# Optimization experiments

Hardware: AMD Instinct MI355X
Metric: run time of the kernel (lower is better)

Reference implementation:

```python
import jax, jax.numpy as jnp
import numpy as np

B, S, S2, NH, H, NKEYS = 2, 4096, 2048, 8, 64, 64


def setup_inputs() -> dict:
    key = jax.random.key(0)
    kq, kk, kv, ki = jax.random.split(key, 4)
    q = jax.random.normal(kq, (B, S2, NH, H), dtype=jnp.float32)
    k = jax.random.normal(kk, (B, S, NH, H), dtype=jnp.float32)
    v = jax.random.normal(kv, (B, S, NH, H), dtype=jnp.float32)
    indices_select = jax.random.randint(ki, (B, S2, NKEYS), 0, S, dtype=jnp.int64)
    return {"q": q, "k": k, "v": v, "indices_select": indices_select}


def reference(q, k, v, indices_select):
    b, s, nh, h = k.shape
    q = q * (h ** -0.5)
    # gather n random keys/values per (batch, query): (b, s2, n, nh, h)
    batch_idx = jnp.arange(b)[:, None, None]
    k_g = k[batch_idx, indices_select]
    v_g = v[batch_idx, indices_select]
    # scores over the n gathered keys, per head: (b, q, k, n)
    A = jnp.einsum('bqnh,bqknh->bqkn', q, k_g)
    A = jax.nn.softmax(A, axis=-2)  # softmax over gathered-key dim (torch dim=-2)
    z = jnp.einsum('bqkn,bqknh->bqnh', A, v_g)
    return z
```

## Files before the change

### kernel.cpp

```cpp
#include <hip/hip_runtime.h>


#define BB 2
#define SS 4096
#define S2V 2048
#define NHV 8
#define HV 64
#define NKV 64

__global__ __launch_bounds__(256)
__attribute__((amdgpu_waves_per_eu(4, 4)))
void rsa_kernel(const float* __restrict__ q, const float* __restrict__ k,
                const float* __restrict__ v, const int* __restrict__ idx,
                float* __restrict__ out) {
    const int lane = threadIdx.x & 63;
    const int w    = threadIdx.x >> 6;
    const int bi   = blockIdx.x;

    const int combo = bi & 15;
    const int b     = combo >> 3;
    const int n     = combo & 7;
    const int qi    = ((bi >> 4) << 2) + w;

    const int g  = lane >> 4;
    const int hc = lane & 15;

    const size_t bq = (size_t)b * S2V + qi;

    const float* qrow = q + (bq * NHV + n) * HV;
    const float4 qv = *(const float4*)(qrow + hc * 4);
    const float4 q4 = make_float4(qv.x * 0.125f, qv.y * 0.125f,
                                  qv.z * 0.125f, qv.w * 0.125f);

    const int my_off = idx[bq * NKV + lane] * (NHV * HV);

    const float* kb = k + ((size_t)b * SS * NHV + n) * HV;
    const float* vb = v + ((size_t)b * SS * NHV + n) * HV;

    float4 kr[16];
#pragma unroll
    for (int it = 0; it < 16; ++it) {
        const int off = __shfl(my_off, it * 4 + g, 64);
        kr[it] = *(const float4*)(kb + off + hc * 4);
    }

    float sc[16];
#pragma unroll
    for (int it = 0; it < 16; ++it) {
        float d = kr[it].x * q4.x + kr[it].y * q4.y
                + kr[it].z * q4.z + kr[it].w * q4.w;
        d += __shfl_xor(d, 1);
        d += __shfl_xor(d, 2);
        d += __shfl_xor(d, 4);
        d += __shfl_xor(d, 8);
        sc[it] = d;
    }

    float4 vr[16];
#pragma unroll
    for (int it = 0; it < 16; ++it) {
        const int off = __shfl(my_off, it * 4 + g, 64);
        vr[it] = *(const float4*)(vb + off + hc * 4);
    }

    float m = sc[0];
#pragma unroll
    for (int it = 1; it < 16; ++it) m = fmaxf(m, sc[it]);
    m = fmaxf(m, __shfl_xor(m, 16));
    m = fmaxf(m, __shfl_xor(m, 32));

    float ssum = 0.f;
#pragma unroll
    for (int it = 0; it < 16; ++it) {
        sc[it] = __expf(sc[it] - m);
        ssum += sc[it];
    }
    ssum += __shfl_xor(ssum, 16);
    ssum += __shfl_xor(ssum, 32);
    const float rs = __frcp_rn(ssum);

    float4 z = make_float4(0.f, 0.f, 0.f, 0.f);
#pragma unroll
    for (int it = 0; it < 16; ++it) {
        const float p = sc[it];
        z.x = fmaf(p, vr[it].x, z.x);
        z.y = fmaf(p, vr[it].y, z.y);
        z.z = fmaf(p, vr[it].z, z.z);
        z.w = fmaf(p, vr[it].w, z.w);
    }
    z.x += __shfl_xor(z.x, 16); z.y += __shfl_xor(z.y, 16);
    z.z += __shfl_xor(z.z, 16); z.w += __shfl_xor(z.w, 16);
    z.x += __shfl_xor(z.x, 32); z.y += __shfl_xor(z.y, 32);
    z.z += __shfl_xor(z.z, 32); z.w += __shfl_xor(z.w, 32);

    if (g == 0) {
        float4 zo = make_float4(z.x * rs, z.y * rs, z.z * rs, z.w * rs);
        *(float4*)(out + (bq * NHV + n) * HV + hc * 4) = zo;
    }
}

extern "C" void kernel_launch(void* const* d_in, const int* in_sizes, int n_in,
                              void* d_out, int out_size, void* d_ws, size_t ws_size,
                              hipStream_t stream) {
    const float* q   = (const float*)d_in[0];
    const float* k   = (const float*)d_in[1];
    const float* v   = (const float*)d_in[2];
    const int*   idx = (const int*)d_in[3];
    float*       out = (float*)d_out;

    const int n_units = BB * S2V * NHV;
    const int blocks  = n_units / 4;
    rsa_kernel<<<blocks, 256, 0, stream>>>(q, k, v, idx, out);
}
```

Measured before the change: 123.8 us.

## Convert K/V to fp16 in workspace before the gather-attention kernel

Adds a pre-pass kernel that converts K and V to fp16 in the workspace buffer. The attention kernel then gathers half-width rows, with 8 lanes per key and 8 elements per lane, and accumulates in fp32. This halves the bytes moved by the random gathers, which dominate the cost. In exchange it adds an extra full read and write pass over K and V every call, and introduces fp16 rounding on the keys and values. A restructured fp32 fallback, which interleaves loads with compute, runs only when the workspace is too small.

```diff
diff --git a/kernel.cpp b/kernel.cpp
--- a/kernel.cpp
+++ b/kernel.cpp
@@ -1,4 +1,5 @@
 #include <hip/hip_runtime.h>
+#include <stdint.h>
 
 
 #define BB 2
@@ -8,11 +9,29 @@
 #define HV 64
 #define NKV 64
 
+typedef _Float16 half_t;
+typedef _Float16 half8 __attribute__((ext_vector_type(8)));
+
+#define NE ((size_t)BB * SS * NHV * HV)
+
 __global__ __launch_bounds__(256)
-__attribute__((amdgpu_waves_per_eu(4, 4)))
-void rsa_kernel(const float* __restrict__ q, const float* __restrict__ k,
-                const float* __restrict__ v, const int* __restrict__ idx,
-                float* __restrict__ out) {
+void cvt_kernel(const float* __restrict__ k, const float* __restrict__ v,
+                half_t* __restrict__ kh, half_t* __restrict__ vh) {
+    const size_t base = ((size_t)blockIdx.x * 256 + threadIdx.x) * 8;
+    const float* src; half_t* dst; size_t off;
+    if (base < NE) { src = k; dst = kh; off = base; }
+    else           { src = v; dst = vh; off = base - NE; }
+    const float4 a = *(const float4*)(src + off);
+    const float4 b = *(const float4*)(src + off + 4);
+    half8 h = { (_Float16)a.x, (_Float16)a.y, (_Float16)a.z, (_Float16)a.w,
+                (_Float16)b.x, (_Float16)b.y, (_Float16)b.z, (_Float16)b.w };
+    *(half8*)(dst + off) = h;
+}
+
+__global__ __launch_bounds__(256)
+void rsa_fp16_kernel(const float* __restrict__ q, const half_t* __restrict__ kh,
+                     const half_t* __restrict__ vh, const int* __restrict__ idx,
+                     float* __restrict__ out) {
     const int lane = threadIdx.x & 63;
     const int w    = threadIdx.x >> 6;
     const int bi   = blockIdx.x;
@@ -22,77 +41,136 @@
     const int n     = combo & 7;
     const int qi    = ((bi >> 4) << 2) + w;
 
+    const int g  = lane >> 3;
+    const int hc = lane & 7;
+
+    const size_t bq = (size_t)b * S2V + qi;
+
+    const float* qrow = q + (bq * NHV + n) * HV;
+    const float4 qa = *(const float4*)(qrow + hc * 8);
+    const float4 qb = *(const float4*)(qrow + hc * 8 + 4);
+    float qf[8] = { qa.x * 0.125f, qa.y * 0.125f, qa.z * 0.125f, qa.w * 0.125f,
+                    qb.x * 0.125f, qb.y * 0.125f, qb.z * 0.125f, qb.w * 0.125f };
+
+    const int my_off = idx[bq * NKV + lane] * (NHV * HV);
+
+    const half_t* kb = kh + ((size_t)b * SS * NHV + n) * HV;
+    const half_t* vb = vh + ((size_t)b * SS * NHV + n) * HV;
+
+    float sc[8];
+#pragma unroll
+    for (int it = 0; it < 8; ++it) {
+        const int off = __shfl(my_off, it * 8 + g, 64);
+        const half8 kk = *(const half8*)(kb + off + hc * 8);
+        float d = 0.f;
+#pragma unroll
+        for (int j = 0; j < 8; ++j) d = fmaf((float)kk[j], qf[j], d);
+        d += __shfl_xor(d, 1);
+        d += __shfl_xor(d, 2);
+        d += __shfl_xor(d, 4);
+        sc[it] = d;
+    }
+
+    float m = sc[0];
+#pragma unroll
+    for (int it = 1; it < 8; ++it) m = fmaxf(m, sc[it]);
+    m = fmaxf(m, __shfl_xor(m, 8));
+    m = fmaxf(m, __shfl_xor(m, 16));
+    m = fmaxf(m, __shfl_xor(m, 32));
+
+    float ssum = 0.f;
+#pragma unroll
+    for (int it = 0; it < 8; ++it) {
+        sc[it] = __expf(sc[it] - m);
+        ssum += sc[it];
+    }
+    ssum += __shfl_xor(ssum, 8);
+    ssum += __shfl_xor(ssum, 16);
+    ssum += __shfl_xor(ssum, 32);
+    const float rs = __frcp_rn(ssum);
+
+    float za[8] = {0.f, 0.f, 0.f, 0.f, 0.f, 0.f, 0.f, 0.f};
+#pragma unroll
+    for (int it = 0; it < 8; ++it) {
+        const int off = __shfl(my_off, it * 8 + g, 64);
+        const half8 vv = *(const half8*)(vb + off + hc * 8);
+        const float p = sc[it];
+#pragma unroll
+        for (int j = 0; j < 8; ++j) za[j] = fmaf(p, (float)vv[j], za[j]);
+    }
+#pragma unroll
+    for (int j = 0; j < 8; ++j) {
+        za[j] += __shfl_xor(za[j], 8);
+        za[j] += __shfl_xor(za[j], 16);
+        za[j] += __shfl_xor(za[j], 32);
+    }
+
+    if (g == 0) {
+        float* orow = out + (bq * NHV + n) * HV + hc * 8;
+        float4 o1 = make_float4(za[0] * rs, za[1] * rs, za[2] * rs, za[3] * rs);
+        float4 o2 = make_float4(za[4] * rs, za[5] * rs, za[6] * rs, za[7] * rs);
+        *(float4*)(orow)     = o1;
+        *(float4*)(orow + 4) = o2;
+    }
+}
+
+__global__ __launch_bounds__(256)
+void rsa_fp32_kernel(const float* __restrict__ q, const float* __restrict__ k,
+                     const float* __restrict__ v, const int* __restrict__ idx,
+                     float* __restrict__ out) {
+    const int lane = threadIdx.x & 63;
+    const int w    = threadIdx.x >> 6;
+    const int bi   = blockIdx.x;
+    const int combo = bi & 15;
+    const int b     = combo >> 3;
+    const int n     = combo & 7;
+    const int qi    = ((bi >> 4) << 2) + w;
     const int g  = lane >> 4;
     const int hc = lane & 15;
-
     const size_t bq = (size_t)b * S2V + qi;
-
     const float* qrow = q + (bq * NHV + n) * HV;
     const float4 qv = *(const float4*)(qrow + hc * 4);
     const float4 q4 = make_float4(qv.x * 0.125f, qv.y * 0.125f,
                                   qv.z * 0.125f, qv.w * 0.125f);
-
     const int my_off = idx[bq * NKV + lane] * (NHV * HV);
-
     const float* kb = k + ((size_t)b * SS * NHV + n) * HV;
     const float* vb = v + ((size_t)b * SS * NHV + n) * HV;
-
-    float4 kr[16];
+    float sc[16];
 #pragma unroll
     for (int it = 0; it < 16; ++it) {
         const int off = __shfl(my_off, it * 4 + g, 64);
-        kr[it] = *(const float4*)(kb + off + hc * 4);
-    }
-
-    float sc[16];
-#pragma unroll
-    for (int it = 0; it < 16; ++it) {
-        float d = kr[it].x * q4.x + kr[it].y * q4.y
-                + kr[it].z * q4.z + kr[it].w * q4.w;
+        const float4 k4 = *(const float4*)(kb + off + hc * 4);
+        float d = k4.x * q4.x + k4.y * q4.y + k4.z * q4.z + k4.w * q4.w;
         d += __shfl_xor(d, 1);
         d += __shfl_xor(d, 2);
         d += __shfl_xor(d, 4);
         d += __shfl_xor(d, 8);
         sc[it] = d;
     }
-
-    float4 vr[16];
-#pragma unroll
-    for (int it = 0; it < 16; ++it) {
-        const int off = __shfl(my_off, it * 4 + g, 64);
-        vr[it] = *(const float4*)(vb + off + hc * 4);
-    }
-
     float m = sc[0];
 #pragma unroll
     for (int it = 1; it < 16; ++it) m = fmaxf(m, sc[it]);
     m = fmaxf(m, __shfl_xor(m, 16));
     m = fmaxf(m, __shfl_xor(m, 32));
-
     float ssum = 0.f;
 #pragma unroll
-    for (int it = 0; it < 16; ++it) {
-        sc[it] = __expf(sc[it] - m);
-        ssum += sc[it];
-    }
+    for (int it = 0; it < 16; ++it) { sc[it] = __expf(sc[it] - m); ssum += sc[it]; }
     ssum += __shfl_xor(ssum, 16);
     ssum += __shfl_xor(ssum, 32);
     const float rs = __frcp_rn(ssum);
-
     float4 z = make_float4(0.f, 0.f, 0.f, 0.f);
 #pragma unroll
     for (int it = 0; it < 16; ++it) {
+        const int off = __shfl(my_off, it * 4 + g, 64);
+        const float4 v4 = *(const float4*)(vb + off + hc * 4);
         const float p = sc[it];
-        z.x = fmaf(p, vr[it].x, z.x);
-        z.y = fmaf(p, vr[it].y, z.y);
-        z.z = fmaf(p, vr[it].z, z.z);
-        z.w = fmaf(p, vr[it].w, z.w);
+        z.x = fmaf(p, v4.x, z.x); z.y = fmaf(p, v4.y, z.y);
+        z.z = fmaf(p, v4.z, z.z); z.w = fmaf(p, v4.w, z.w);
     }
     z.x += __shfl_xor(z.x, 16); z.y += __shfl_xor(z.y, 16);
     z.z += __shfl_xor(z.z, 16); z.w += __shfl_xor(z.w, 16);
     z.x += __shfl_xor(z.x, 32); z.y += __shfl_xor(z.y, 32);
     z.z += __shfl_xor(z.z, 32); z.w += __shfl_xor(z.w, 32);
-
     if (g == 0) {
         float4 zo = make_float4(z.x * rs, z.y * rs, z.z * rs, z.w * rs);
         *(float4*)(out + (bq * NHV + n) * HV + hc * 4) = zo;
@@ -110,5 +188,15 @@
 
     const int n_units = BB * S2V * NHV;
     const int blocks  = n_units / 4;
-    rsa_kernel<<<blocks, 256, 0, stream>>>(q, k, v, idx, out);
-}
+
+    const size_t need = 2 * NE * sizeof(half_t);
+    if (ws_size >= need) {
+        half_t* kh = (half_t*)d_ws;
+        half_t* vh = kh + NE;
+        const int cvt_blocks = (int)(2 * NE / 8 / 256);
+        cvt_kernel<<<cvt_blocks, 256, 0, stream>>>(k, v, kh, vh);
+        rsa_fp16_kernel<<<blocks, 256, 0, stream>>>(q, kh, vh, idx, out);
+    } else {
+        rsa_fp32_kernel<<<blocks, 256, 0, stream>>>(q, k, v, idx, out);
+    }
+}
```

Measured after the change: 113.5 us. 1.09x faster.
